# Performance work log

Hardware: AMD Instinct MI355X
Metric: run time of the kernel (lower is better)

Reference implementation:

```python
import jax, jax.numpy as jnp
import numpy as np

# Regularized layout for the per-batch masked attention:
#   batch_size B=8, each batch has NF=2048 'fill' points followed by NK=4096 'keep' points.
B, NF, NK = 8, 2048, 4096
C_IN, C_KQ, C_OUT = 256, 64, 256


def setup_inputs() -> dict:
    key = jax.random.key(0)
    ks = jax.random.split(key, 7)
    N = B * (NF + NK)
    features = jax.random.normal(ks[0], (N, C_IN), dtype=jnp.float32)
    # keep flag: 0 for fill points, 1 for keep points, per batch (fill-first layout)
    flag = jnp.tile(jnp.concatenate([jnp.zeros(NF, jnp.int32), jnp.ones(NK, jnp.int32)]), B)
    s = 1.0 / np.sqrt(C_IN)
    Wq = jax.random.normal(ks[1], (C_KQ, C_IN), jnp.float32) * s
    bq = jnp.zeros((C_KQ,), jnp.float32)
    Wk = jax.random.normal(ks[2], (C_KQ, C_IN), jnp.float32) * s
    bk = jnp.zeros((C_KQ,), jnp.float32)
    Wv = jax.random.normal(ks[3], (C_OUT, C_IN), jnp.float32) * s
    bv = jnp.zeros((C_OUT,), jnp.float32)
    return {"features": features, "keep_flag": flag,
            "Wq": Wq, "bq": bq, "Wk": Wk, "bk": bk, "Wv": Wv, "bv": bv}


def reference(features, keep_flag, Wq, bq, Wk, bk, Wv, bv):
    # features: [N, C_IN]; keep_flag encodes the fill/keep split, which in this
    # regular layout is: first NF rows of each batch are fill, remaining NK are keep.
    del keep_flag  # structure is encoded in the layout (fill-first per batch)
    f = features.reshape(B, NF + NK, C_IN)
    fill = f[:, :NF]             # [B, NF, C_IN]
    keep = f[:, NF:]             # [B, NK, C_IN]
    q = fill @ Wq.T + bq         # [B, NF, C_KQ]
    k = keep @ Wk.T + bk         # [B, NK, C_KQ]
    v = keep @ Wv.T + bv         # [B, NK, C_OUT]
    ratio = np.sqrt(C_KQ).astype(np.float32)
    scores = jnp.einsum('bfd,bkd->bfk', q, k) / ratio   # [B, NF, NK]
    attn = jax.nn.softmax(scores, axis=-1)
    out_fill = jnp.einsum('bfk,bkc->bfc', attn, v)      # [B, NF, C_OUT]
    # keep rows pass through unchanged (only fill rows are overwritten)
    out = jnp.concatenate([out_fill, keep], axis=1)
    return out.reshape(B * (NF + NK), C_OUT)
```

## Files before the change

### kernel.cpp

```cpp
#include <hip/hip_runtime.h>
#include <hip/hip_bf16.h>

#define BATCHES 8
#define NFILL 2048
#define NKEEP 4096
#define SEQLEN 6144
#define CIN 256
#define CKQ 64
#define COUT 256

#define KSC 0.18033688011112042f
#define KOFF -11.541560327111707f

#define SWZ(r) (((r)&7) << 3)

typedef __bf16 bf16_t;
typedef float f32x4 __attribute__((ext_vector_type(4)));
typedef bf16_t bf16x8 __attribute__((ext_vector_type(8)));
typedef bf16_t bf16x4 __attribute__((ext_vector_type(4)));

__device__ inline void cvt8_store(bf16_t* dst, float4 a, float4 b) {
  bf16x8 v;
  v[0] = (bf16_t)a.x; v[1] = (bf16_t)a.y; v[2] = (bf16_t)a.z; v[3] = (bf16_t)a.w;
  v[4] = (bf16_t)b.x; v[5] = (bf16_t)b.y; v[6] = (bf16_t)b.z; v[7] = (bf16_t)b.w;
  *(bf16x8*)dst = v;
}

__global__ __launch_bounds__(256, 3) void gemm_qkv(
    const float* __restrict__ feat, const float* __restrict__ Wq,
    const float* __restrict__ bq, const float* __restrict__ Wk,
    const float* __restrict__ bk, const float* __restrict__ Wv,
    const float* __restrict__ bv, bf16_t* __restrict__ Qw,
    bf16_t* __restrict__ Kw, bf16_t* __restrict__ Vw,
    float* __restrict__ outp) {
  __shared__ bf16_t Xs[64][256];
  __shared__ bf16_t Ws[2][64][64];

  const int bid = blockIdx.x;
  const bool isQ = bid >= 512;
  const int mb = isQ ? bid - 512 : bid;

  const int t = threadIdx.x;
  const int lane = t & 63;
  const int wv = t >> 6;
  const int l16 = lane & 15;
  const int quad = lane >> 4;

  const int lr = t >> 2;
  const int koff = (t & 3) << 4;
  const int swl = SWZ(lr);
  const int swr = SWZ(l16);

  const int mrow = mb * 64 + lr;
  const int rpb_shift = isQ ? 11 : 12;
  const int batch = mrow >> rpb_shift;
  const int ridx = mrow & ((1 << rpb_shift) - 1);
  const int row_off = isQ ? 0 : NFILL;
  const long grow = (long)(batch * SEQLEN + row_off + ridx);
  const float* xptr = feat + grow * CIN;
  float4* orow = (float4*)(outp + grow * COUT);

  const int NT = isQ ? 1 : 5;
  const int G = NT * 4;
  const float* w0src = isQ ? Wq : Wk;

#define WCHUNK_PTR(g)                                                        \
  (((g) < 4 ? w0src : Wv + (long)((((g) >> 2) - 1) * 64) * CIN) +            \
   (long)lr * CIN + ((g)&3) * 64 + koff)

  float4 wr[2][4];
  {
    const float* wp = WCHUNK_PTR(0);
#pragma unroll
    for (int s = 0; s < 4; s++) wr[0][s] = *(const float4*)(wp + s * 4);
  }

#pragma unroll
  for (int j = 0; j < 4; j++) {
    const int c = koff + j * 64;
    float4 x0 = *(const float4*)(xptr + c);
    float4 x1 = *(const float4*)(xptr + c + 4);
    float4 x2 = *(const float4*)(xptr + c + 8);
    float4 x3 = *(const float4*)(xptr + c + 12);
    cvt8_store(&Xs[lr][c ^ swl], x0, x1);
    cvt8_store(&Xs[lr][(c + 8) ^ swl], x2, x3);
    if (!isQ) {
      orow[(c >> 2) + 0] = x0;
      orow[(c >> 2) + 1] = x1;
      orow[(c >> 2) + 2] = x2;
      orow[(c >> 2) + 3] = x3;
    }
  }
  cvt8_store(&Ws[0][lr][koff ^ swl], wr[0][0], wr[0][1]);
  cvt8_store(&Ws[0][lr][(koff + 8) ^ swl], wr[0][2], wr[0][3]);
  {
    const float* wp = WCHUNK_PTR(1);
#pragma unroll
    for (int s = 0; s < 4; s++) wr[1][s] = *(const float4*)(wp + s * 4);
  }
  asm volatile("s_waitcnt lgkmcnt(0)\n\ts_barrier" ::: "memory");

  const int vb = (mb * 64) >> 12;
  const int key0base = (mb * 64) & 4095;

  f32x4 acc[4];
#pragma unroll 1
  for (int nt = 0; nt < NT; nt++) {
#pragma unroll
    for (int nb = 0; nb < 4; nb++) acc[nb] = f32x4{0.f, 0.f, 0.f, 0.f};

#pragma unroll
    for (int kc = 0; kc < 4; kc++) {
      const int g = nt * 4 + kc;
      const int cb = g & 1;
      const bool last = (g + 1 == G);

      if (!last) {
        cvt8_store(&Ws[cb ^ 1][lr][koff ^ swl], wr[cb ^ 1][0], wr[cb ^ 1][1]);
        cvt8_store(&Ws[cb ^ 1][lr][(koff + 8) ^ swl], wr[cb ^ 1][2], wr[cb ^ 1][3]);
      }
      if (g + 2 < G) {
        const float* wp = WCHUNK_PTR(g + 2);
#pragma unroll
        for (int s = 0; s < 4; s++) wr[cb][s] = *(const float4*)(wp + s * 4);
      }

      if (nt == 0) {
#pragma unroll
        for (int ks = 0; ks < 2; ks++) {
          bf16x8 afrag = *(const bf16x8*)
              &Xs[wv * 16 + l16][(kc * 64) + ((ks * 32 + quad * 8) ^ swr)];
#pragma unroll
          for (int nb = 0; nb < 4; nb++) {
            bf16x8 bfrag = *(const bf16x8*)
                &Ws[cb][nb * 16 + l16][(ks * 32 + quad * 8) ^ swr];
            acc[nb] = __builtin_amdgcn_mfma_f32_16x16x32_bf16(afrag, bfrag, acc[nb], 0, 0, 0);
          }
        }
      } else {
#pragma unroll
        for (int ks = 0; ks < 2; ks++) {
          bf16x8 xfrag = *(const bf16x8*)
              &Xs[wv * 16 + l16][(kc * 64) + ((ks * 32 + quad * 8) ^ swr)];
#pragma unroll
          for (int nb = 0; nb < 4; nb++) {
            bf16x8 wfrag = *(const bf16x8*)
                &Ws[cb][nb * 16 + l16][(ks * 32 + quad * 8) ^ swr];
            acc[nb] = __builtin_amdgcn_mfma_f32_16x16x32_bf16(wfrag, xfrag, acc[nb], 0, 0, 0);
          }
        }
      }

      if (!last)
        asm volatile("s_waitcnt lgkmcnt(0)\n\ts_barrier" ::: "memory");
    }

    if (nt == 0) {
      const float* bias = isQ ? bq : bk;
      bf16_t* op = isQ ? Qw : Kw;
#pragma unroll
      for (int nb = 0; nb < 4; nb++) {
        const int n = nb * 16 + l16;
        const float bb = bias[n];
#pragma unroll
        for (int r = 0; r < 4; r++) {
          const int m = mb * 64 + wv * 16 + quad * 4 + r;
          op[(long)m * CKQ + n] = (bf16_t)(acc[nb][r] + bb);
        }
      }
    } else {
      const int n0 = (nt - 1) * 64;
#pragma unroll
      for (int nb = 0; nb < 4; nb++) {
        f32x4 bbv = *(const f32x4*)&bv[n0 + nb * 16 + quad * 4];
        bf16_t* vdst = Vw +
                       ((long)(vb * COUT + n0 + nb * 16 + quad * 4)) * NKEEP +
                       key0base + wv * 16 + l16;
#pragma unroll
        for (int r = 0; r < 4; r++)
          vdst[(long)r * NKEEP] = (bf16_t)(acc[nb][r] + bbv[r]);
      }
    }
  }
#undef WCHUNK_PTR
}

__global__ __launch_bounds__(256) void attn_kernel(
    const bf16_t* __restrict__ Q, const bf16_t* __restrict__ K,
    const bf16_t* __restrict__ Vt, float* __restrict__ outp) {
  __shared__ bf16_t Ks[2][64][64];
  __shared__ bf16_t Ps[64][64];
  __shared__ float Lsh[64];

  const int b = blockIdx.x & 7;
  const int qt = blockIdx.x >> 3;
  const int t = threadIdx.x;
  const int lane = t & 63;
  const int wv = t >> 6;
  const int l16 = lane & 15;
  const int quad = lane >> 4;

  const int krow = t >> 2;
  const int kcol = (t & 3) << 4;
  const int swk = SWZ(krow);
  const int swr = SWZ(l16);

  const bf16_t* kbase = K + (long)b * NKEEP * CKQ;
  const int c0 = wv * 64;
  const bf16_t* vlane =
      Vt + ((long)(b * COUT + c0 + l16)) * NKEEP + quad * 8;

  bf16x8 qfrag[2];
  {
    const bf16_t* qrow = Q + ((long)(b * NFILL + qt * 64 + wv * 16 + l16)) * CKQ;
#pragma unroll
    for (int ks = 0; ks < 2; ks++)
      qfrag[ks] = *(const bf16x8*)(qrow + ks * 32 + quad * 8);
  }

  f32x4 oacc[4][4];
#pragma unroll
  for (int m = 0; m < 4; m++)
#pragma unroll
    for (int ct = 0; ct < 4; ct++) oacc[m][ct] = f32x4{0.f, 0.f, 0.f, 0.f};
  float rsum = 0.f;

  uint4 kreg0, kreg1;
  bf16x8 vA[8], vB[8];

  {
    const bf16_t* ksrc = kbase + (long)krow * CKQ + kcol;
    uint4 k0 = *(const uint4*)ksrc;
    uint4 k1 = *(const uint4*)(ksrc + 8);
#pragma unroll
    for (int ct = 0; ct < 4; ct++)
#pragma unroll
      for (int ks = 0; ks < 2; ks++)
        vA[ct * 2 + ks] = *(const bf16x8*)(vlane + (long)ct * 16 * NKEEP + ks * 32);
    *(uint4*)&Ks[0][krow][kcol ^ swk] = k0;
    *(uint4*)&Ks[0][krow][(kcol + 8) ^ swk] = k1;
  }

#define ATTN_TILE(BUF, VCUR, VNEXT, TV)                                         \
  {                                                                             \
    __syncthreads(); \
    const int tn = ((TV) + 1 < 64) ? (TV) + 1 : 63;                             \
    {                                                                           \
      const bf16_t* ksrc = kbase + ((long)(tn * 64 + krow)) * CKQ + kcol;       \
      kreg0 = *(const uint4*)ksrc;                                              \
      kreg1 = *(const uint4*)(ksrc + 8);                                        \
      const bf16_t* vsrc = vlane + (long)tn * 64;                               \
      _Pragma("unroll") for (int ct = 0; ct < 4; ct++)                          \
          _Pragma("unroll") for (int ks = 0; ks < 2; ks++)                      \
              VNEXT[ct * 2 + ks] =                                              \
          *(const bf16x8*)(vsrc + (long)ct * 16 * NKEEP + ks * 32);             \
    }                                                                           \
    f32x4 sacc[4];   \
    _Pragma("unroll") for (int kb = 0; kb < 4; kb++)                            \
        sacc[kb] = f32x4{0.f, 0.f, 0.f, 0.f};                                   \
    _Pragma("unroll") for (int ks = 0; ks < 2; ks++) {                          \
      _Pragma("unroll") for (int kb = 0; kb < 4; kb++) {                        \
        bf16x8 kfrag = *(const bf16x8*)                                         \
            &Ks[BUF][kb * 16 + l16][(ks * 32 + quad * 8) ^ swr];                \
        sacc[kb] = __builtin_amdgcn_mfma_f32_16x16x32_bf16(kfrag, qfrag[ks],    \
                                                           sacc[kb], 0, 0, 0); \
      }                                                                         \
    }                                                                           \
    _Pragma("unroll") for (int kb = 0; kb < 4; kb++) {                          \
      const float e0 = __builtin_exp2f(fmaf(sacc[kb][0], KSC, KOFF));           \
      const float e1 = __builtin_exp2f(fmaf(sacc[kb][1], KSC, KOFF));           \
      const float e2 = __builtin_exp2f(fmaf(sacc[kb][2], KSC, KOFF));           \
      const float e3 = __builtin_exp2f(fmaf(sacc[kb][3], KSC, KOFF));           \
      rsum += (e0 + e1) + (e2 + e3);                                            \
      bf16x4 pk;                                                                \
      pk[0] = (bf16_t)e0; pk[1] = (bf16_t)e1;                                   \
      pk[2] = (bf16_t)e2; pk[3] = (bf16_t)e3;                                   \
      *(bf16x4*)&Ps[wv * 16 + l16][(kb * 16 + quad * 4) ^ swr] = pk;            \
    }                                                                           \
    asm volatile("s_waitcnt lgkmcnt(0)\n\ts_barrier" ::: "memory");      \
    _Pragma("unroll") for (int ks = 0; ks < 2; ks++) {                          \
      _Pragma("unroll") for (int m = 0; m < 4; m++) {                           \
        bf16x8 pfrag = *(const bf16x8*)                                         \
            &Ps[m * 16 + l16][(ks * 32 + quad * 8) ^ swr];                      \
        _Pragma("unroll") for (int ct = 0; ct < 4; ct++)                        \
            oacc[m][ct] = __builtin_amdgcn_mfma_f32_16x16x32_bf16(              \
                pfrag, VCUR[ct * 2 + ks], oacc[m][ct], 0, 0, 0);                \
      }                                                                         \
    }                                                                           \
    *(uint4*)&Ks[BUF ^ 1][krow][kcol ^ swk] = kreg0;                            \
    *(uint4*)&Ks[BUF ^ 1][krow][(kcol + 8) ^ swk] = kreg1;                      \
  }

#pragma unroll 1
  for (int tv = 0; tv < 64; tv += 2) {
    ATTN_TILE(0, vA, vB, tv)
    ATTN_TILE(1, vB, vA, tv + 1)
  }
#undef ATTN_TILE

  rsum += __shfl_xor(rsum, 16, 64);
  rsum += __shfl_xor(rsum, 32, 64);
  if (quad == 0) Lsh[wv * 16 + l16] = rsum;
  __syncthreads();

  float rl[4][4];
#pragma unroll
  for (int m = 0; m < 4; m++)
#pragma unroll
    for (int r = 0; r < 4; r++) rl[m][r] = 1.0f / Lsh[m * 16 + quad * 4 + r];

  const long obase = ((long)(b * SEQLEN + qt * 64)) * COUT + c0;
#pragma unroll
  for (int m = 0; m < 4; m++)
#pragma unroll
    for (int ct = 0; ct < 4; ct++)
#pragma unroll
      for (int r = 0; r < 4; r++)
        outp[obase + (long)(m * 16 + quad * 4 + r) * COUT + ct * 16 + l16] =
            oacc[m][ct][r] * rl[m][r];
}

extern "C" void kernel_launch(void* const* d_in, const int* in_sizes, int n_in,
                              void* d_out, int out_size, void* d_ws, size_t ws_size,
                              hipStream_t stream) {
  const float* feat = (const float*)d_in[0];
  const float* Wq = (const float*)d_in[2];
  const float* bq = (const float*)d_in[3];
  const float* Wk = (const float*)d_in[4];
  const float* bk = (const float*)d_in[5];
  const float* Wv = (const float*)d_in[6];
  const float* bv = (const float*)d_in[7];
  float* outp = (float*)d_out;

  bf16_t* Qw = (bf16_t*)d_ws;
  bf16_t* Kw = Qw + (size_t)BATCHES * NFILL * CKQ;
  bf16_t* Vw = Kw + (size_t)BATCHES * NKEEP * CKQ;

  gemm_qkv<<<dim3(768), 256, 0, stream>>>(feat, Wq, bq, Wk, bk, Wv, bv,
                                          Qw, Kw, Vw, outp);
  attn_kernel<<<dim3(NFILL / 64 * BATCHES), 256, 0, stream>>>(Qw, Kw, Vw, outp);
}
```

Before: 209.4 us.

## Double attention key tile to 128 and load V for the current tile

The attention loop now processes 128 keys per iteration instead of 64, halving the number of barriers and loop iterations. K is still double-buffered in shared memory, but V is no longer prefetched one tile ahead: each iteration loads the current tile's 16 V fragments into registers. This gives fewer synchronisations and more MFMA work per barrier, at the cost of more LDS per block and V global-load latency now sitting in the critical path.

```diff
diff --git a/kernel.cpp b/kernel.cpp
--- a/kernel.cpp
+++ b/kernel.cpp
@@ -188,8 +188,8 @@
 __global__ __launch_bounds__(256) void attn_kernel(
     const bf16_t* __restrict__ Q, const bf16_t* __restrict__ K,
     const bf16_t* __restrict__ Vt, float* __restrict__ outp) {
-  __shared__ bf16_t Ks[2][64][64];
-  __shared__ bf16_t Ps[64][64];
+  __shared__ bf16_t Ks[2][128][64];
+  __shared__ bf16_t Ps[64][128];
   __shared__ float Lsh[64];
 
   const int b = blockIdx.x & 7;
@@ -200,8 +200,8 @@
   const int l16 = lane & 15;
   const int quad = lane >> 4;
 
-  const int krow = t >> 2;
-  const int kcol = (t & 3) << 4;
+  const int krow = t >> 1;
+  const int kcolh = (t & 1) << 5;
   const int swk = SWZ(krow);
   const int swr = SWZ(l16);
 
@@ -225,76 +225,73 @@
     for (int ct = 0; ct < 4; ct++) oacc[m][ct] = f32x4{0.f, 0.f, 0.f, 0.f};
   float rsum = 0.f;
 
-  uint4 kreg0, kreg1;
-  bf16x8 vA[8], vB[8];
+  uint4 kreg[4];
+  bf16x8 vcur[16];
 
   {
-    const bf16_t* ksrc = kbase + (long)krow * CKQ + kcol;
-    uint4 k0 = *(const uint4*)ksrc;
-    uint4 k1 = *(const uint4*)(ksrc + 8);
-#pragma unroll
-    for (int ct = 0; ct < 4; ct++)
-#pragma unroll
-      for (int ks = 0; ks < 2; ks++)
-        vA[ct * 2 + ks] = *(const bf16x8*)(vlane + (long)ct * 16 * NKEEP + ks * 32);
-    *(uint4*)&Ks[0][krow][kcol ^ swk] = k0;
-    *(uint4*)&Ks[0][krow][(kcol + 8) ^ swk] = k1;
-  }
-
-#define ATTN_TILE(BUF, VCUR, VNEXT, TV)                                         \
+    const bf16_t* ksrc = kbase + (long)krow * CKQ + kcolh;
+#pragma unroll
+    for (int j = 0; j < 4; j++)
+      *(uint4*)&Ks[0][krow][(kcolh + j * 8) ^ swk] = *(const uint4*)(ksrc + j * 8);
+  }
+
+#define ATTN_TILE(BUF, TV)                                                      \
   {                                                                             \
-    __syncthreads(); \
-    const int tn = ((TV) + 1 < 64) ? (TV) + 1 : 63;                             \
-    {                                                                           \
-      const bf16_t* ksrc = kbase + ((long)(tn * 64 + krow)) * CKQ + kcol;       \
-      kreg0 = *(const uint4*)ksrc;                                              \
-      kreg1 = *(const uint4*)(ksrc + 8);                                        \
-      const bf16_t* vsrc = vlane + (long)tn * 64;                               \
+    __syncthreads();                \
+    const int tn = ((TV) + 1 < 32) ? (TV) + 1 : 31;                             \
+    {       \
+      const bf16_t* ksrc = kbase + ((long)(tn * 128 + krow)) * CKQ + kcolh;     \
+      _Pragma("unroll") for (int j = 0; j < 4; j++)                             \
+          kreg[j] = *(const uint4*)(ksrc + j * 8);                              \
+      const bf16_t* vsrc = vlane + (long)(TV) * 128;                            \
       _Pragma("unroll") for (int ct = 0; ct < 4; ct++)                          \
-          _Pragma("unroll") for (int ks = 0; ks < 2; ks++)                      \
-              VNEXT[ct * 2 + ks] =                                              \
-          *(const bf16x8*)(vsrc + (long)ct * 16 * NKEEP + ks * 32);             \
+          _Pragma("unroll") for (int vks = 0; vks < 4; vks++)                   \
+              vcur[ct * 4 + vks] =                                              \
+          *(const bf16x8*)(vsrc + (long)ct * 16 * NKEEP + vks * 32);            \
     }                                                                           \
-    f32x4 sacc[4];   \
-    _Pragma("unroll") for (int kb = 0; kb < 4; kb++)                            \
-        sacc[kb] = f32x4{0.f, 0.f, 0.f, 0.f};                                   \
-    _Pragma("unroll") for (int ks = 0; ks < 2; ks++) {                          \
+                                \
+    _Pragma("unroll") for (int h = 0; h < 2; h++) {                             \
+      f32x4 sacc[4]; \
+      _Pragma("unroll") for (int kb = 0; kb < 4; kb++)                          \
+          sacc[kb] = f32x4{0.f, 0.f, 0.f, 0.f};                                 \
+      _Pragma("unroll") for (int ks = 0; ks < 2; ks++) {                        \
+        _Pragma("unroll") for (int kb = 0; kb < 4; kb++) {                      \
+          bf16x8 kfrag = *(const bf16x8*)                                       \
+              &Ks[BUF][(h * 4 + kb) * 16 + l16][(ks * 32 + quad * 8) ^ swr];    \
+          sacc[kb] = __builtin_amdgcn_mfma_f32_16x16x32_bf16(                   \
+              kfrag, qfrag[ks], sacc[kb], 0, 0, 0);                             \
+        }                                                                       \
+      }                                                                         \
       _Pragma("unroll") for (int kb = 0; kb < 4; kb++) {                        \
-        bf16x8 kfrag = *(const bf16x8*)                                         \
-            &Ks[BUF][kb * 16 + l16][(ks * 32 + quad * 8) ^ swr];                \
-        sacc[kb] = __builtin_amdgcn_mfma_f32_16x16x32_bf16(kfrag, qfrag[ks],    \
-                                                           sacc[kb], 0, 0, 0); \
+        const float e0 = __builtin_exp2f(fmaf(sacc[kb][0], KSC, KOFF));         \
+        const float e1 = __builtin_exp2f(fmaf(sacc[kb][1], KSC, KOFF));         \
+        const float e2 = __builtin_exp2f(fmaf(sacc[kb][2], KSC, KOFF));         \
+        const float e3 = __builtin_exp2f(fmaf(sacc[kb][3], KSC, KOFF));         \
+        rsum += (e0 + e1) + (e2 + e3);                                          \
+        bf16x4 pk;                                                              \
+        pk[0] = (bf16_t)e0; pk[1] = (bf16_t)e1;                                 \
+        pk[2] = (bf16_t)e2; pk[3] = (bf16_t)e3;                                 \
+        *(bf16x4*)&Ps[wv * 16 + l16][((h * 4 + kb) * 16 + quad * 4) ^ swr] = pk;\
       }                                                                         \
     }                                                                           \
-    _Pragma("unroll") for (int kb = 0; kb < 4; kb++) {                          \
-      const float e0 = __builtin_exp2f(fmaf(sacc[kb][0], KSC, KOFF));           \
-      const float e1 = __builtin_exp2f(fmaf(sacc[kb][1], KSC, KOFF));           \
-      const float e2 = __builtin_exp2f(fmaf(sacc[kb][2], KSC, KOFF));           \
-      const float e3 = __builtin_exp2f(fmaf(sacc[kb][3], KSC, KOFF));           \
-      rsum += (e0 + e1) + (e2 + e3);                                            \
-      bf16x4 pk;                                                                \
-      pk[0] = (bf16_t)e0; pk[1] = (bf16_t)e1;                                   \
-      pk[2] = (bf16_t)e2; pk[3] = (bf16_t)e3;                                   \
-      *(bf16x4*)&Ps[wv * 16 + l16][(kb * 16 + quad * 4) ^ swr] = pk;            \
-    }                                                                           \
-    asm volatile("s_waitcnt lgkmcnt(0)\n\ts_barrier" ::: "memory");      \
-    _Pragma("unroll") for (int ks = 0; ks < 2; ks++) {                          \
+    asm volatile("s_waitcnt lgkmcnt(0)\n\ts_barrier" ::: "memory");  \
+    _Pragma("unroll") for (int pks = 0; pks < 4; pks++) {                       \
       _Pragma("unroll") for (int m = 0; m < 4; m++) {                           \
         bf16x8 pfrag = *(const bf16x8*)                                         \
-            &Ps[m * 16 + l16][(ks * 32 + quad * 8) ^ swr];                      \
+            &Ps[m * 16 + l16][(pks * 32 + quad * 8) ^ swr];                     \
         _Pragma("unroll") for (int ct = 0; ct < 4; ct++)                        \
             oacc[m][ct] = __builtin_amdgcn_mfma_f32_16x16x32_bf16(              \
-                pfrag, VCUR[ct * 2 + ks], oacc[m][ct], 0, 0, 0);                \
+                pfrag, vcur[ct * 4 + pks], oacc[m][ct], 0, 0, 0);               \
       }                                                                         \
     }                                                                           \
-    *(uint4*)&Ks[BUF ^ 1][krow][kcol ^ swk] = kreg0;                            \
-    *(uint4*)&Ks[BUF ^ 1][krow][(kcol + 8) ^ swk] = kreg1;                      \
+    _Pragma("unroll") for (int j = 0; j < 4; j++)                               \
+        *(uint4*)&Ks[BUF ^ 1][krow][(kcolh + j * 8) ^ swk] = kreg[j];           \
   }
 
 #pragma unroll 1
-  for (int tv = 0; tv < 64; tv += 2) {
-    ATTN_TILE(0, vA, vB, tv)
-    ATTN_TILE(1, vB, vA, tv + 1)
+  for (int tv = 0; tv < 32; tv += 2) {
+    ATTN_TILE(0, tv)
+    ATTN_TILE(1, tv + 1)
   }
 #undef ATTN_TILE
 
```

Result: slower. 220.8 us (+5.4%).
